# Kernel tuning notes

Measured on AMD Instinct MI355X. Metric: run time of the kernel, lower is better.

Reference implementation:

```python
import jax, jax.numpy as jnp
import numpy as np

D_MODEL = 1024
NUM_HEADS = 16
D_K = D_MODEL // NUM_HEADS
B, S = 4, 2048


def setup_inputs() -> dict:
    key = jax.random.key(0)
    ks = jax.random.split(key, 11)
    scale = 1.0 / np.sqrt(D_MODEL)
    inp = {
        'query': jax.random.normal(ks[0], (B, S, D_MODEL), dtype=jnp.float32),
        'key':   jax.random.normal(ks[1], (B, S, D_MODEL), dtype=jnp.float32),
        'value': jax.random.normal(ks[2], (B, S, D_MODEL), dtype=jnp.float32),
        'Wq': jax.random.normal(ks[3], (D_MODEL, D_MODEL), dtype=jnp.float32) * scale,
        'bq': jnp.zeros((D_MODEL,), dtype=jnp.float32),
        'Wk': jax.random.normal(ks[4], (D_MODEL, D_MODEL), dtype=jnp.float32) * scale,
        'bk': jnp.zeros((D_MODEL,), dtype=jnp.float32),
        'Wv': jax.random.normal(ks[5], (D_MODEL, D_MODEL), dtype=jnp.float32) * scale,
        'bv': jnp.zeros((D_MODEL,), dtype=jnp.float32),
        'Wo': jax.random.normal(ks[6], (D_MODEL, D_MODEL), dtype=jnp.float32) * scale,
        'bo': jnp.zeros((D_MODEL,), dtype=jnp.float32),
    }
    return inp


def reference(query, key, value, Wq, bq, Wk, bk, Wv, bv, Wo, bo):
    b, sq, _ = query.shape
    sk = key.shape[1]
    # projections (torch Linear: x @ W.T + b; here W stored as [in, out])
    Q = query @ Wq + bq
    K = key @ Wk + bk
    V = value @ Wv + bv
    # split heads: [b, h, s, d_k]
    Q = Q.reshape(b, sq, NUM_HEADS, D_K).transpose(0, 2, 1, 3)
    K = K.reshape(b, sk, NUM_HEADS, D_K).transpose(0, 2, 1, 3)
    V = V.reshape(b, sk, NUM_HEADS, D_K).transpose(0, 2, 1, 3)
    # scaled dot-product attention (full [b,h,sq,sk] scores, as in source)
    scores = jnp.einsum('bhqd,bhkd->bhqk', Q, K) / jnp.sqrt(jnp.float32(D_K))
    attn = jax.nn.softmax(scores, axis=-1)
    out = jnp.einsum('bhqk,bhkd->bhqd', attn, V)
    out = out.transpose(0, 2, 1, 3).reshape(b, sq, D_MODEL)
    return out @ Wo + bo
```

## Files before the change

### kernel.cpp

```cpp
#include <hip/hip_runtime.h>
#include <hip/hip_bf16.h>
#include <stdint.h>

typedef __bf16 bf16x8 __attribute__((ext_vector_type(8)));
typedef __bf16 bf16x4 __attribute__((ext_vector_type(4)));
typedef float  f32x4  __attribute__((ext_vector_type(4)));
typedef unsigned short u16;

#define D_MODEL 1024
#define NUM_HEADS 16
#define DK 64
#define BATCH 4
#define SEQ 2048
#define M_TOTAL (BATCH*SEQ)
#define MD ((size_t)M_TOTAL * D_MODEL)
#define QK_SCALE 0.18033688011112042f

static __device__ __forceinline__ u16 f2bf(float f) {
    __bf16 h = (__bf16)f;
    return __builtin_bit_cast(u16, h);
}

#define ASYNC16(gptr, lptr) __builtin_amdgcn_global_load_lds( \
    (const __attribute__((address_space(1))) unsigned*)(uintptr_t)(gptr), \
    (__attribute__((address_space(3))) unsigned*)(unsigned)(uintptr_t)(lptr), 16, 0, 0)

__global__ void detect_dtype(const u16* __restrict__ q, unsigned* __restrict__ flag) {
    __shared__ int sh[256];
    int cnt = 0;
    for (int i = threadIdx.x; i < 8192; i += 256) {
        u16 v = q[2 * i];
        int e = (v >> 7) & 0xFF;
        if (e >= 100 && e <= 134) cnt++;
    }
    sh[threadIdx.x] = cnt;
    __syncthreads();
    for (int s = 128; s > 0; s >>= 1) {
        if (threadIdx.x < s) sh[threadIdx.x] += sh[threadIdx.x + s];
        __syncthreads();
    }
    if (threadIdx.x == 0) *flag = (sh[0] > 4096) ? 1u : 0u;
}

__global__ __launch_bounds__(256) void convert_bf16(
    const u16* __restrict__ q, const u16* __restrict__ k, const u16* __restrict__ v,
    u16* __restrict__ CVT, const unsigned* __restrict__ flagp)
{
    if (*flagp != 0) return;
    const int z = blockIdx.y;
    const float* src = (const float*)((z == 0) ? q : (z == 1) ? k : v);
    u16* dst = CVT + (size_t)z * MD;
    const size_t stride = (size_t)gridDim.x * 256 * 8;
    for (size_t base = ((size_t)blockIdx.x * 256 + threadIdx.x) * 8; base < MD; base += stride) {
        float4 f0 = *(const float4*)(src + base);
        float4 f1 = *(const float4*)(src + base + 4);
        bf16x8 p;
        p[0] = (__bf16)f0.x; p[1] = (__bf16)f0.y; p[2] = (__bf16)f0.z; p[3] = (__bf16)f0.w;
        p[4] = (__bf16)f1.x; p[5] = (__bf16)f1.y; p[6] = (__bf16)f1.z; p[7] = (__bf16)f1.w;
        *(bf16x8*)(dst + base) = p;
    }
}

__global__ void transpose_w(const u16* __restrict__ W0, const u16* __restrict__ W1,
                            const u16* __restrict__ W2, const u16* __restrict__ W3,
                            u16* __restrict__ WT, const unsigned* __restrict__ flagp) {
    __shared__ u16 tile[32][33];
    const u16* W = (blockIdx.z == 0) ? W0 : (blockIdx.z == 1) ? W1 : (blockIdx.z == 2) ? W2 : W3;
    u16* T = WT + (size_t)blockIdx.z * D_MODEL * D_MODEL;
    bool is_bf16 = (*flagp != 0);
    int x = threadIdx.x, y0 = threadIdx.y;
    int bx = blockIdx.x * 32, by = blockIdx.y * 32;
    if (is_bf16) {
#pragma unroll
        for (int i = 0; i < 4; i++) {
            int y = y0 + i * 8;
            tile[y][x] = W[(size_t)(by + y) * D_MODEL + bx + x];
        }
    } else {
        const float* Wf = (const float*)W;
#pragma unroll
        for (int i = 0; i < 4; i++) {
            int y = y0 + i * 8;
            tile[y][x] = f2bf(Wf[(size_t)(by + y) * D_MODEL + bx + x]);
        }
    }
    __syncthreads();
#pragma unroll
    for (int i = 0; i < 4; i++) {
        int y = y0 + i * 8;
        T[(size_t)(bx + y) * D_MODEL + by + x] = tile[x][y];
    }
}

__global__ __launch_bounds__(256) void gemm_qkv(
    const u16* __restrict__ qin, const u16* __restrict__ kin, const u16* __restrict__ vin,
    const u16* __restrict__ CVT, const u16* __restrict__ WT,
    const u16* __restrict__ bq, const u16* __restrict__ bk, const u16* __restrict__ bv,
    u16* __restrict__ Qp, u16* __restrict__ Kp, u16* __restrict__ VpT,
    const unsigned* __restrict__ flagp)
{
    __shared__ __align__(16) u16 As[128 * 64];
    __shared__ __align__(16) u16 Bs[128 * 64];

    const int id  = blockIdx.x;
    const int wg  = (id & 7) * 192 + (id >> 3);
    const int z   = wg >> 9;
    const int rr  = wg & 511;
    const int m_blk = (rr >> 3) * 128;
    const int n_blk = (rr & 7) * 128;

    const bool is_bf16 = (*flagp != 0);
    const u16* A = is_bf16 ? ((z == 0) ? qin : (z == 1) ? kin : vin)
                           : (CVT + (size_t)z * MD);
    const u16* W    = WT + (size_t)z * 1048576;
    const u16* bias = (z == 0) ? bq : (z == 1) ? bk : bv;
    u16* C          = (z == 0) ? Qp : (z == 1) ? Kp : VpT;
    const float oscale = (z == 0) ? QK_SCALE : 1.0f;

    const int tid  = threadIdx.x;
    const int lane = tid & 63, w = tid >> 6;
    const int quad = lane >> 4, l15 = lane & 15;
    const int swz  = l15 & 7;
    const int wm = w >> 1, wn = w & 1;

    const int lrow = lane >> 3;
    const int ug   = (lane & 7) ^ lrow;

    f32x4 acc[4][4] = {};

    for (int k0 = 0; k0 < D_MODEL; k0 += 64) {
#pragma unroll
        for (int i = 0; i < 4; i++) {
            const int c = w * 4 + i;
            ASYNC16(A + (size_t)(m_blk + c * 8 + lrow) * D_MODEL + k0 + ug * 8, &As[c * 512]);
            ASYNC16(W + (size_t)(n_blk + c * 8 + lrow) * D_MODEL + k0 + ug * 8, &Bs[c * 512]);
        }
        __syncthreads();

        bf16x8 a[4][2], b[4][2];
#pragma unroll
        for (int mf = 0; mf < 4; mf++)
#pragma unroll
            for (int ks = 0; ks < 2; ks++)
                a[mf][ks] = *(const bf16x8*)&As[(size_t)(wm * 64 + mf * 16 + l15) * 64
                                                + (((ks * 4 + quad) ^ swz) * 8)];
#pragma unroll
        for (int nf = 0; nf < 4; nf++)
#pragma unroll
            for (int ks = 0; ks < 2; ks++)
                b[nf][ks] = *(const bf16x8*)&Bs[(size_t)(wn * 64 + nf * 16 + l15) * 64
                                                + (((ks * 4 + quad) ^ swz) * 8)];
#pragma unroll
        for (int mf = 0; mf < 4; mf++)
#pragma unroll
            for (int nf = 0; nf < 4; nf++)
#pragma unroll
                for (int ks = 0; ks < 2; ks++)
                    acc[mf][nf] = __builtin_amdgcn_mfma_f32_16x16x32_bf16(
                        a[mf][ks], b[nf][ks], acc[mf][nf], 0, 0, 0);
        __syncthreads();
    }

#pragma unroll
    for (int nf = 0; nf < 4; nf++) {
        const int n = n_blk + wn * 64 + nf * 16 + l15;
        const float bvf = is_bf16 ? (float)((const __bf16*)bias)[n] : ((const float*)bias)[n];
#pragma unroll
        for (int mf = 0; mf < 4; mf++) {
            const int mrow = m_blk + wm * 64 + mf * 16 + quad * 4;
            if (z == 2) {
                const int bb = mrow >> 11, s = mrow & 2047;
                ushort4 pk;
                pk.x = f2bf(acc[mf][nf][0] + bvf);
                pk.y = f2bf(acc[mf][nf][1] + bvf);
                pk.z = f2bf(acc[mf][nf][2] + bvf);
                pk.w = f2bf(acc[mf][nf][3] + bvf);
                *(ushort4*)(C + (size_t)bb * D_MODEL * SEQ + (size_t)n * SEQ + s) = pk;
            } else {
#pragma unroll
                for (int r = 0; r < 4; r++)
                    C[(size_t)(mrow + r) * D_MODEL + n] = f2bf((acc[mf][nf][r] + bvf) * oscale);
            }
        }
    }
}

__global__ __launch_bounds__(256) void gemm_o(
    const u16* __restrict__ A, const u16* __restrict__ WT,
    const u16* __restrict__ bias, u16* __restrict__ C,
    const unsigned* __restrict__ flagp)
{
    __shared__ __align__(16) u16 As[64 * 32];
    __shared__ __align__(16) u16 Bs[128 * 32];
    const int id  = blockIdx.x;
    const int xcd = id & 7, j = id >> 3;
    const int by  = xcd * 16 + (j >> 3);
    const int bx  = j & 7;

    const int tid  = threadIdx.x;
    const int lane = tid & 63, w = tid >> 6;
    const int quad = lane >> 4, l15 = lane & 15;
    const int wm = w >> 1, wn = w & 1;
    const int m_blk = by * 64, n_blk = bx * 128;
    const bool is_bf16 = (*flagp != 0);

    f32x4 acc[2][4] = {};
    const int srow = lane >> 2, skp = (lane & 3) * 8;

    for (int k0 = 0; k0 < D_MODEL; k0 += 32) {
#pragma unroll
        for (int i = 0; i < 3; i++) {
            int c = w * 3 + i;
            if (c < 4)
                ASYNC16(A  + (size_t)(m_blk + c * 16 + srow) * D_MODEL + k0 + skp, &As[c * 512]);
            else
                ASYNC16(WT + (size_t)(n_blk + (c - 4) * 16 + srow) * D_MODEL + k0 + skp, &Bs[(c - 4) * 512]);
        }
        __syncthreads();

        bf16x8 af[2], bg[4];
#pragma unroll
        for (int sm = 0; sm < 2; sm++)
            af[sm] = *(const bf16x8*)&As[(wm * 32 + sm * 16 + l15) * 32 + quad * 8];
#pragma unroll
        for (int sn = 0; sn < 4; sn++)
            bg[sn] = *(const bf16x8*)&Bs[(wn * 64 + sn * 16 + l15) * 32 + quad * 8];
#pragma unroll
        for (int sm = 0; sm < 2; sm++)
#pragma unroll
            for (int sn = 0; sn < 4; sn++)
                acc[sm][sn] = __builtin_amdgcn_mfma_f32_16x16x32_bf16(af[sm], bg[sn], acc[sm][sn], 0, 0, 0);
        __syncthreads();
    }

#pragma unroll
    for (int sn = 0; sn < 4; sn++) {
        int n = n_blk + wn * 64 + sn * 16 + l15;
        float bvf = is_bf16 ? (float)((const __bf16*)bias)[n] : ((const float*)bias)[n];
#pragma unroll
        for (int sm = 0; sm < 2; sm++) {
            int mrow = m_blk + wm * 32 + sm * 16 + quad * 4;
            if (!is_bf16) {
                float* Cf = (float*)C;
#pragma unroll
                for (int r = 0; r < 4; r++)
                    Cf[(size_t)(mrow + r) * D_MODEL + n] = acc[sm][sn][r] + bvf;
            } else {
#pragma unroll
                for (int r = 0; r < 4; r++)
                    C[(size_t)(mrow + r) * D_MODEL + n] = f2bf(acc[sm][sn][r] + bvf);
            }
        }
    }
}

__global__ __launch_bounds__(512, 4) void attn_kernel(
    const u16* __restrict__ Qp, const u16* __restrict__ Kp,
    const u16* __restrict__ VpT, u16* __restrict__ AO)
{
    __shared__ __align__(16) u16 Ks[2][64 * 64];
    __shared__ __align__(16) u16 Vs[2][64 * 64];
    __shared__ __align__(16) u16 Ps[8][32][68];
    const int id  = blockIdx.x;
    const int xcd = id & 7, j = id >> 3;
    const int bh  = xcd * 8 + (j >> 3);
    const int qx  = j & 7;

    const int tid  = threadIdx.x;
    const int lane = tid & 63, w = tid >> 6;
    const int quad = lane >> 4, l15 = lane & 15;
    const int b = bh >> 4, h = bh & 15;
    const int q_base = qx * 256 + w * 32;

    bf16x8 bQ[2][2];
#pragma unroll
    for (int sn = 0; sn < 2; sn++)
#pragma unroll
        for (int ds = 0; ds < 2; ds++)
            bQ[sn][ds] = *(const bf16x8*)(Qp + (size_t)(b * SEQ + q_base + sn * 16 + l15) * D_MODEL
                                              + h * DK + ds * 32 + quad * 8);

    f32x4 OT[2][4] = {};
    f32x4 OTs[2]  = {};
    bf16x8 aOnes;
#pragma unroll
    for (int i = 0; i < 8; i++) aOnes[i] = (__bf16)1.0f;

    const u16* Kbase = Kp  + (size_t)(b * SEQ) * D_MODEL + h * DK;
    const u16* Vbase = VpT + (size_t)b * D_MODEL * SEQ + (size_t)(h * DK) * SEQ;

    const int lrow = lane >> 3;
    const int ug   = (lane & 7) ^ lrow;
    const int swz  = l15 & 7;

    auto issue_tile = [&](int key0, int bf) {
        ASYNC16(Kbase + (size_t)(key0 + w * 8 + lrow) * D_MODEL + ug * 8, &Ks[bf][w * 512]);
        ASYNC16(Vbase + (size_t)(w * 8 + lrow) * SEQ + key0 + ug * 8,     &Vs[bf][w * 512]);
    };

    issue_tile(0, 0);
    __syncthreads();

    for (int t = 0; t < SEQ / 64; t++) {
        const int cur = t & 1;
        if (t + 1 < SEQ / 64) issue_tile((t + 1) * 64, cur ^ 1);

#pragma unroll
        for (int kc = 0; kc < 4; kc++) {
            const int krow = (kc * 16 + l15) * 64;
            bf16x8 k0 = *(const bf16x8*)&Ks[cur][krow + ((quad ^ swz) * 8)];
            bf16x8 k1 = *(const bf16x8*)&Ks[cur][krow + (((4 + quad) ^ swz) * 8)];
#pragma unroll
            for (int sn = 0; sn < 2; sn++) {
                f32x4 s = {};
                s = __builtin_amdgcn_mfma_f32_16x16x32_bf16(k0, bQ[sn][0], s, 0, 0, 0);
                s = __builtin_amdgcn_mfma_f32_16x16x32_bf16(k1, bQ[sn][1], s, 0, 0, 0);
                bf16x4 pk;
                pk[0] = (__bf16)__builtin_amdgcn_exp2f(s[0]);
                pk[1] = (__bf16)__builtin_amdgcn_exp2f(s[1]);
                pk[2] = (__bf16)__builtin_amdgcn_exp2f(s[2]);
                pk[3] = (__bf16)__builtin_amdgcn_exp2f(s[3]);
                *(bf16x4*)&Ps[w][sn * 16 + l15][kc * 16 + quad * 4] = pk;
            }
        }

#pragma unroll
        for (int kc2 = 0; kc2 < 2; kc2++) {
            bf16x8 bP0 = *(const bf16x8*)&Ps[w][l15][kc2 * 32 + quad * 8];
            bf16x8 bP1 = *(const bf16x8*)&Ps[w][16 + l15][kc2 * 32 + quad * 8];
            OTs[0] = __builtin_amdgcn_mfma_f32_16x16x32_bf16(aOnes, bP0, OTs[0], 0, 0, 0);
            OTs[1] = __builtin_amdgcn_mfma_f32_16x16x32_bf16(aOnes, bP1, OTs[1], 0, 0, 0);
#pragma unroll
            for (int nd = 0; nd < 4; nd++) {
                bf16x8 aV = *(const bf16x8*)&Vs[cur][(nd * 16 + l15) * 64
                                                    + (((kc2 * 4 + quad) ^ swz) * 8)];
                OT[0][nd] = __builtin_amdgcn_mfma_f32_16x16x32_bf16(aV, bP0, OT[0][nd], 0, 0, 0);
                OT[1][nd] = __builtin_amdgcn_mfma_f32_16x16x32_bf16(aV, bP1, OT[1][nd], 0, 0, 0);
            }
        }
        __syncthreads();
    }

#pragma unroll
    for (int sn = 0; sn < 2; sn++) {
        float rl = 1.0f / OTs[sn][0];
        size_t rowbase = (size_t)(b * SEQ + q_base + sn * 16 + l15) * D_MODEL + h * DK;
#pragma unroll
        for (int nd = 0; nd < 4; nd++) {
            ushort4 pk;
            pk.x = f2bf(OT[sn][nd][0] * rl);
            pk.y = f2bf(OT[sn][nd][1] * rl);
            pk.z = f2bf(OT[sn][nd][2] * rl);
            pk.w = f2bf(OT[sn][nd][3] * rl);
            *(ushort4*)(AO + rowbase + nd * 16 + quad * 4) = pk;
        }
    }
}

extern "C" void kernel_launch(void* const* d_in, const int* in_sizes, int n_in,
                              void* d_out, int out_size, void* d_ws, size_t ws_size,
                              hipStream_t stream) {
    const u16* q  = (const u16*)d_in[0];
    const u16* k  = (const u16*)d_in[1];
    const u16* v  = (const u16*)d_in[2];
    const u16* Wq = (const u16*)d_in[3];
    const u16* bq = (const u16*)d_in[4];
    const u16* Wk = (const u16*)d_in[5];
    const u16* bk = (const u16*)d_in[6];
    const u16* Wv = (const u16*)d_in[7];
    const u16* bv = (const u16*)d_in[8];
    const u16* Wo = (const u16*)d_in[9];
    const u16* bo = (const u16*)d_in[10];

    u16* ws   = (u16*)d_ws;
    unsigned* flagp = (unsigned*)ws;
    u16* WT   = ws + 16;
    u16* Qp   = WT + (size_t)4 * 1024 * 1024;
    u16* Kp   = Qp + MD;
    u16* VpT  = Kp + MD;
    u16* CVT  = VpT + MD;
    u16* AO   = CVT;

    detect_dtype<<<1, 256, 0, stream>>>(q, flagp);
    convert_bf16<<<dim3(1024, 3), 256, 0, stream>>>(q, k, v, CVT, flagp);
    transpose_w<<<dim3(32, 32, 4), dim3(32, 8), 0, stream>>>(Wq, Wk, Wv, Wo, WT, flagp);
    gemm_qkv<<<1536, 256, 0, stream>>>(q, k, v, CVT, WT, bq, bk, bv, Qp, Kp, VpT, flagp);
    attn_kernel<<<512, 512, 0, stream>>>(Qp, Kp, VpT, AO);
    gemm_o<<<1024, 256, 0, stream>>>(AO, WT + 3 * 1048576, bo, (u16*)d_out, flagp);
}
```

Before: 381.7 us.

## Enlarge output-projection GEMM tile to 128x128x64 with XOR-swizzled LDS

The output-projection GEMM moves from 64x128 tiles with K-step 32 to 128x128 tiles with K-step 64, so each wave computes a 64x64 sub-tile. LDS rows use an XOR swizzle on 16-byte chunks to avoid bank conflicts, and the block-to-XCD mapping is reworked for the 512-block grid. The goal is more data reuse per load and fewer barriers per K. In exchange it uses more registers and LDS and launches fewer blocks, which lowers occupancy.

Result: faster. 367.0 us (-3.8%).

```diff
diff --git a/kernel.cpp b/kernel.cpp
--- a/kernel.cpp
+++ b/kernel.cpp
@@ -190,65 +190,76 @@
     const u16* __restrict__ bias, u16* __restrict__ C,
     const unsigned* __restrict__ flagp)
 {
-    __shared__ __align__(16) u16 As[64 * 32];
-    __shared__ __align__(16) u16 Bs[128 * 32];
+    __shared__ __align__(16) u16 As[128 * 64];
+    __shared__ __align__(16) u16 Bs[128 * 64];
+
     const int id  = blockIdx.x;
-    const int xcd = id & 7, j = id >> 3;
-    const int by  = xcd * 16 + (j >> 3);
-    const int bx  = j & 7;
+    const int wg  = (id & 7) * 64 + (id >> 3);
+    const int m_blk = (wg >> 3) * 128;
+    const int n_blk = (wg & 7) * 128;
+
+    const bool is_bf16 = (*flagp != 0);
 
     const int tid  = threadIdx.x;
     const int lane = tid & 63, w = tid >> 6;
     const int quad = lane >> 4, l15 = lane & 15;
+    const int swz  = l15 & 7;
     const int wm = w >> 1, wn = w & 1;
-    const int m_blk = by * 64, n_blk = bx * 128;
-    const bool is_bf16 = (*flagp != 0);
-
-    f32x4 acc[2][4] = {};
-    const int srow = lane >> 2, skp = (lane & 3) * 8;
-
-    for (int k0 = 0; k0 < D_MODEL; k0 += 32) {
-#pragma unroll
-        for (int i = 0; i < 3; i++) {
-            int c = w * 3 + i;
-            if (c < 4)
-                ASYNC16(A  + (size_t)(m_blk + c * 16 + srow) * D_MODEL + k0 + skp, &As[c * 512]);
-            else
-                ASYNC16(WT + (size_t)(n_blk + (c - 4) * 16 + srow) * D_MODEL + k0 + skp, &Bs[(c - 4) * 512]);
-        }
-        __syncthreads();
-
-        bf16x8 af[2], bg[4];
-#pragma unroll
-        for (int sm = 0; sm < 2; sm++)
-            af[sm] = *(const bf16x8*)&As[(wm * 32 + sm * 16 + l15) * 32 + quad * 8];
-#pragma unroll
-        for (int sn = 0; sn < 4; sn++)
-            bg[sn] = *(const bf16x8*)&Bs[(wn * 64 + sn * 16 + l15) * 32 + quad * 8];
-#pragma unroll
-        for (int sm = 0; sm < 2; sm++)
-#pragma unroll
-            for (int sn = 0; sn < 4; sn++)
-                acc[sm][sn] = __builtin_amdgcn_mfma_f32_16x16x32_bf16(af[sm], bg[sn], acc[sm][sn], 0, 0, 0);
-        __syncthreads();
-    }
-
-#pragma unroll
-    for (int sn = 0; sn < 4; sn++) {
-        int n = n_blk + wn * 64 + sn * 16 + l15;
-        float bvf = is_bf16 ? (float)((const __bf16*)bias)[n] : ((const float*)bias)[n];
-#pragma unroll
-        for (int sm = 0; sm < 2; sm++) {
-            int mrow = m_blk + wm * 32 + sm * 16 + quad * 4;
+
+    const int lrow = lane >> 3;
+    const int ug   = (lane & 7) ^ lrow;
+
+    f32x4 acc[4][4] = {};
+
+    for (int k0 = 0; k0 < D_MODEL; k0 += 64) {
+#pragma unroll
+        for (int i = 0; i < 4; i++) {
+            const int c = w * 4 + i;
+            ASYNC16(A  + (size_t)(m_blk + c * 8 + lrow) * D_MODEL + k0 + ug * 8, &As[c * 512]);
+            ASYNC16(WT + (size_t)(n_blk + c * 8 + lrow) * D_MODEL + k0 + ug * 8, &Bs[c * 512]);
+        }
+        __syncthreads();
+
+        bf16x8 a[4][2], b[4][2];
+#pragma unroll
+        for (int mf = 0; mf < 4; mf++)
+#pragma unroll
+            for (int ks = 0; ks < 2; ks++)
+                a[mf][ks] = *(const bf16x8*)&As[(size_t)(wm * 64 + mf * 16 + l15) * 64
+                                                + (((ks * 4 + quad) ^ swz) * 8)];
+#pragma unroll
+        for (int nf = 0; nf < 4; nf++)
+#pragma unroll
+            for (int ks = 0; ks < 2; ks++)
+                b[nf][ks] = *(const bf16x8*)&Bs[(size_t)(wn * 64 + nf * 16 + l15) * 64
+                                                + (((ks * 4 + quad) ^ swz) * 8)];
+#pragma unroll
+        for (int mf = 0; mf < 4; mf++)
+#pragma unroll
+            for (int nf = 0; nf < 4; nf++)
+#pragma unroll
+                for (int ks = 0; ks < 2; ks++)
+                    acc[mf][nf] = __builtin_amdgcn_mfma_f32_16x16x32_bf16(
+                        a[mf][ks], b[nf][ks], acc[mf][nf], 0, 0, 0);
+        __syncthreads();
+    }
+
+#pragma unroll
+    for (int nf = 0; nf < 4; nf++) {
+        const int n = n_blk + wn * 64 + nf * 16 + l15;
+        const float bvf = is_bf16 ? (float)((const __bf16*)bias)[n] : ((const float*)bias)[n];
+#pragma unroll
+        for (int mf = 0; mf < 4; mf++) {
+            const int mrow = m_blk + wm * 64 + mf * 16 + quad * 4;
             if (!is_bf16) {
                 float* Cf = (float*)C;
 #pragma unroll
                 for (int r = 0; r < 4; r++)
-                    Cf[(size_t)(mrow + r) * D_MODEL + n] = acc[sm][sn][r] + bvf;
+                    Cf[(size_t)(mrow + r) * D_MODEL + n] = acc[mf][nf][r] + bvf;
             } else {
 #pragma unroll
                 for (int r = 0; r < 4; r++)
-                    C[(size_t)(mrow + r) * D_MODEL + n] = f2bf(acc[sm][sn][r] + bvf);
+                    C[(size_t)(mrow + r) * D_MODEL + n] = f2bf(acc[mf][nf][r] + bvf);
             }
         }
     }
@@ -386,5 +397,5 @@
     transpose_w<<<dim3(32, 32, 4), dim3(32, 8), 0, stream>>>(Wq, Wk, Wv, Wo, WT, flagp);
     gemm_qkv<<<1536, 256, 0, stream>>>(q, k, v, CVT, WT, bq, bk, bv, Qp, Kp, VpT, flagp);
     attn_kernel<<<512, 512, 0, stream>>>(Qp, Kp, VpT, AO);
-    gemm_o<<<1024, 256, 0, stream>>>(AO, WT + 3 * 1048576, bo, (u16*)d_out, flagp);
-}
+    gemm_o<<<512, 256, 0, stream>>>(AO, WT + 3 * 1048576, bo, (u16*)d_out, flagp);
+}
```
